# Optimization experiments

Hardware: AMD Instinct MI355X
Metric: run time of the kernel (lower is better)

## Reference

```python
import jax, jax.numpy as jnp
import numpy as np

GRID = 32            # grid_size -> num_locs = 1024
H, W = 8, 32         # ray panorama height/width
N_ANGLES = 360       # binned_rays: one bin per rounded degree


def _circ_conv(x, w, b, pad):
    # Conv2d with padding_mode='circular' (NCHW, OIHW)
    if pad > 0:
        x = jnp.pad(x, ((0, 0), (0, 0), (pad, pad), (pad, pad)), mode='wrap')
    y = jax.lax.conv_general_dilated(x, w, (1, 1), 'VALID',
                                     dimension_numbers=('NCHW', 'OIHW', 'NCHW'))
    return y + b[None, :, None, None]


def setup_inputs() -> dict:
    key = jax.random.key(0)
    ks = jax.random.split(key, 8)
    B, N, F, Co = 2, 20, 128, 64
    bbox = jax.random.uniform(ks[0], (B, 4), dtype=jnp.float32)
    near_locs = jax.random.uniform(ks[1], (B, N, 2), dtype=jnp.float32)
    near_feats = jax.random.normal(ks[2], (B, N, F, H, W), dtype=jnp.float32)
    overhead_feat = jax.random.normal(ks[3], (B, Co, GRID, GRID), dtype=jnp.float32)
    rays = jax.random.normal(ks[4], (N_ANGLES, 3, H, W), dtype=jnp.float32)
    cin = 8  # 1 dist + 3 orient + 2 pano stats + 2 overhead stats
    W1 = jax.random.normal(ks[5], (1, cin, 3, 3), dtype=jnp.float32) * 0.1
    b1 = jnp.zeros((1,), jnp.float32)
    W2 = jax.random.normal(ks[6], (1, cin, 5, 5), dtype=jnp.float32) * 0.1
    b2 = jnp.zeros((1,), jnp.float32)
    Wf = jax.random.normal(ks[7], (1, 2, 1, 1), dtype=jnp.float32) * 0.1
    bf = jnp.zeros((1,), jnp.float32)
    return dict(bbox=bbox, near_locs=near_locs, near_feats=near_feats,
                overhead_feat=overhead_feat, rays=rays,
                W1=W1, b1=b1, W2=W2, b2=b2, Wf=Wf, bf=bf)


def _grid_helper(bbox, near_locs):
    # grid-cell centers from bbox; D = euclidean dist, theta = bearing in [0, 2pi)
    ys = jnp.linspace(bbox[0], bbox[2], GRID)
    xs = jnp.linspace(bbox[1], bbox[3], GRID)
    gy, gx = jnp.meshgrid(ys, xs, indexing='ij')
    centers = jnp.stack([gy.ravel(), gx.ravel()], -1)              # [L,2]
    diff = near_locs[None, :, :] - centers[:, None, :]             # [L,N,2]
    D = jnp.sqrt(jnp.sum(diff * diff, -1))                         # [L,N]
    theta = jnp.mod(jnp.arctan2(diff[..., 1], diff[..., 0]), 2.0 * jnp.pi)
    return D, theta


def _one(bbox, near_locs, near_feats, overhead_feat, rays, W1, b1, W2, b2, Wf, bf):
    N, F = near_feats.shape[:2]
    L = GRID * GRID
    D, theta = _grid_helper(bbox, near_locs)
    theta_inds = jnp.mod(jnp.round(jnp.rad2deg(theta)).astype(jnp.int32), N_ANGLES)
    orientation = rays[theta_inds.reshape(-1)].reshape(L, N, 3, H, W)  # irregular gather
    distance = jnp.broadcast_to(D[:, :, None, None, None], (L, N, 1, H, W))
    # panorama stats: max/mean over channel dim of pano features
    pano_stats = jnp.stack([near_feats.max(1), near_feats.mean(1)], 1)  # [N,2,H,W]
    x_pano = jnp.broadcast_to(pano_stats[None], (L, N, 2, H, W))
    # overhead stats: flatten spatial -> (L, Co), max/mean over channels
    ov = overhead_feat.reshape(overhead_feat.shape[0], -1).T            # [L, Co]
    ov_stats = jnp.stack([ov.max(1), ov.mean(1)], 1)                    # [L,2]
    x_ov = jnp.broadcast_to(ov_stats[:, None, :, None, None], (L, N, 2, H, W))
    inp = jnp.concatenate([distance, orientation, x_pano, x_ov], 2)     # [L,N,8,H,W]
    x = inp.reshape(L * N, 8, H, W)
    c1 = _circ_conv(x, W1, b1, 1)
    c2 = _circ_conv(x, W2, b2, 2)
    fused = jnp.concatenate([c1, c2], 1)                                # [L*N,2,H,W]
    logits = _circ_conv(fused, Wf, bf, 0).reshape(L, N, H, W)
    weight = jax.nn.softmax(logits.reshape(L, -1), axis=1).reshape(L, N, H, W)
    tmp_feats = jnp.transpose(near_feats, (0, 2, 3, 1))                 # [N,H,W,F]
    grid_feats = jnp.einsum('pxyf,spxy->sf', tmp_feats, weight)         # [L,F]
    return (grid_feats.reshape(GRID, GRID, F),
            weight.reshape(GRID, GRID, N, H, W))


def reference(bbox, near_locs, near_feats, overhead_feat, rays, W1, b1, W2, b2, Wf, bf):
    fn = jax.vmap(_one, in_axes=(0, 0, 0, 0, None, None, None, None, None, None, None))
    return fn(bbox, near_locs, near_feats, overhead_feat, rays, W1, b1, W2, b2, Wf, bf)
```

## Files before the change

kernel.cpp:

```cpp
#include <hip/hip_runtime.h>
#include <hip/hip_fp16.h>
#include <math.h>

#define HH 8
#define WW 32
#define HW 256
#define NN 20
#define FF 128
#define LL 1024
#define AA 360
#define CO 64
#define KK 5120
#define KS 8
#define KC 640
#define BM 32
#define BK 64

#define OFF_LPANO      (AA*HW)
#define OFF_OV(B)      (OFF_LPANO + (B)*NN*HW)
#define OFF_SCAL(B)    (OFF_OV(B) + (B)*LL*2)
#define OFF_BASE(B)    (OFF_SCAL(B) + 8)
#define OFF_IDX(B)     (OFF_BASE(B) + (B)*LL*NN)
#define OFF_BT(B)      (((OFF_IDX(B) + (B)*LL*NN + 7)/8)*8)
#define OFF_CP(B)      (OFF_BT(B) + (B)*FF*KK/2)

typedef __attribute__((ext_vector_type(8))) _Float16 f16x8;
typedef __attribute__((ext_vector_type(4))) _Float16 f16x4;
typedef __attribute__((ext_vector_type(4))) float f32x4;

__global__ __launch_bounds__(256)
void k1_pre(const float* __restrict__ rays, const float* __restrict__ feats,
            const float* __restrict__ overhead,
            const float* __restrict__ W1, const float* __restrict__ b1,
            const float* __restrict__ W2, const float* __restrict__ b2,
            const float* __restrict__ Wf, const float* __restrict__ bfp,
            float* __restrict__ ws, int B)
{
    const int bid = blockIdx.x, tid = threadIdx.x;
    const float wf0 = Wf[0], wf1 = Wf[1];

    if (bid < AA) {
        __shared__ float s[3*HW];
        for (int c = 0; c < 3; ++c) s[c*HW + tid] = rays[(bid*3 + c)*HW + tid];
        __syncthreads();
        const int h = tid >> 5, w = tid & 31;
        float c1 = 0.f, c2 = 0.f;
        #pragma unroll
        for (int c = 0; c < 3; ++c) {
            #pragma unroll
            for (int ky = 0; ky < 3; ++ky)
                #pragma unroll
                for (int kx = 0; kx < 3; ++kx)
                    c1 += W1[(1+c)*9 + ky*3 + kx] *
                          s[c*HW + (((h+ky+7)&7)<<5) + ((w+kx+31)&31)];
            #pragma unroll
            for (int ky = 0; ky < 5; ++ky)
                #pragma unroll
                for (int kx = 0; kx < 5; ++kx)
                    c2 += W2[(1+c)*25 + ky*5 + kx] *
                          s[c*HW + (((h+ky+6)&7)<<5) + ((w+kx+30)&31)];
        }
        ws[bid*HW + tid] = wf0*c1 + wf1*c2;
        return;
    }

    const int pb = bid - AA;
    if (pb < B*NN) {
        __shared__ float p[2*HW];
        const float* fp = feats + (size_t)pb * FF * HW + tid;
        float mx = -INFINITY; double sm = 0.0;
        for (int f = 0; f < FF; ++f) {
            float v = fp[(size_t)f * HW];
            mx = fmaxf(mx, v); sm += (double)v;
        }
        p[tid]      = mx;
        p[HW + tid] = (float)(sm / 128.0);
        __syncthreads();
        const int h = tid >> 5, w = tid & 31;
        float c1 = 0.f, c2 = 0.f;
        #pragma unroll
        for (int c = 0; c < 2; ++c) {
            #pragma unroll
            for (int ky = 0; ky < 3; ++ky)
                #pragma unroll
                for (int kx = 0; kx < 3; ++kx)
                    c1 += W1[(4+c)*9 + ky*3 + kx] *
                          p[c*HW + (((h+ky+7)&7)<<5) + ((w+kx+31)&31)];
            #pragma unroll
            for (int ky = 0; ky < 5; ++ky)
                #pragma unroll
                for (int kx = 0; kx < 5; ++kx)
                    c2 += W2[(4+c)*25 + ky*5 + kx] *
                          p[c*HW + (((h+ky+6)&7)<<5) + ((w+kx+30)&31)];
        }
        ws[OFF_LPANO + pb*HW + tid] = wf0*c1 + wf1*c2;
        return;
    }

    const int ob = bid - AA - B*NN;
    if (ob < B*4) {
        const int t = ob*256 + tid;
        const int b = t >> 10, l = t & 1023;
        const float* op = overhead + (size_t)b*CO*LL + l;
        float mx = -INFINITY; double sm = 0.0;
        for (int c = 0; c < CO; ++c) {
            float v = op[(size_t)c*LL];
            mx = fmaxf(mx, v); sm += (double)v;
        }
        ws[OFF_OV(B) + t*2]     = mx;
        ws[OFF_OV(B) + t*2 + 1] = (float)(sm / 64.0);
        return;
    }

    if (tid == 0) {
        double s10=0, s16=0, s17=0, s20=0, s26=0, s27=0;
        for (int i = 0; i < 9;  ++i) { s10 += W1[i]; s16 += W1[54+i];  s17 += W1[63+i]; }
        for (int i = 0; i < 25; ++i) { s20 += W2[i]; s26 += W2[150+i]; s27 += W2[175+i]; }
        ws[OFF_SCAL(B)+0] = (float)(wf0*s10 + wf1*s20);
        ws[OFF_SCAL(B)+1] = (float)(wf0*s16 + wf1*s26);
        ws[OFF_SCAL(B)+2] = (float)(wf0*s17 + wf1*s27);
        ws[OFF_SCAL(B)+3] = wf0*b1[0] + wf1*b2[0] + bfp[0];
    }
}

__global__ __launch_bounds__(256)
void k2_geom(const float* __restrict__ bbox, const float* __restrict__ locs,
             float* __restrict__ ws, int B)
{
    const int t = blockIdx.x*256 + threadIdx.x;
    if (t >= B*LL*NN) return;
    const int b = t / (LL*NN), r = t % (LL*NN), l = r / NN, n = r % NN;
    const int iy = l >> 5, ix = l & 31;
    const double y0 = (double)bbox[b*4+0], x0 = (double)bbox[b*4+1];
    const double y1 = (double)bbox[b*4+2], x1 = (double)bbox[b*4+3];
    const double cy = y0 + (double)iy * (y1 - y0) / 31.0;
    const double cx = x0 + (double)ix * (x1 - x0) / 31.0;
    const double d0 = (double)locs[(b*NN+n)*2+0] - cy;
    const double d1 = (double)locs[(b*NN+n)*2+1] - cx;
    const double D  = sqrt(d0*d0 + d1*d1);
    double th = atan2(d1, d0);
    const double TWO_PI = 6.283185307179586476925286766559;
    th -= TWO_PI * floor(th / TWO_PI);
    const double deg = th * 57.295779513082320876798154814105;
    int k = (int)llrint(deg);
    int idx = k % 360; if (idx < 0) idx += 360;

    const float Cd  = ws[OFF_SCAL(B)+0], Com = ws[OFF_SCAL(B)+1];
    const float Cov = ws[OFF_SCAL(B)+2], Cb  = ws[OFF_SCAL(B)+3];
    const int bl = b*LL + l;
    const float bv = (float)(Cd * D) + Com*ws[OFF_OV(B)+bl*2]
                   + Cov*ws[OFF_OV(B)+bl*2+1] + Cb;
    ws[OFF_BASE(B) + t] = bv;
    ((int*)(ws + OFF_IDX(B)))[t] = idx;
}

__global__ __launch_bounds__(256)
void k2b_bt(const float* __restrict__ feats, float* __restrict__ ws, int B)
{
    const int NG_PER_B = NN*FF*64;
    const int g = blockIdx.x*256 + threadIdx.x;
    if (g >= B*NG_PER_B) return;
    const int b = g / NG_PER_B;
    const int r = g - b*NG_PER_B;
    const int n = r / (FF*64);
    const int r2 = r % (FF*64);
    const int f = r2 >> 6;
    const int hw0 = (r2 & 63) << 2;
    const float4 v = *(const float4*)(feats + ((size_t)((b*NN + n)*FF + f))*HW + hw0);
    f16x4 h;
    h[0] = (_Float16)v.x; h[1] = (_Float16)v.y;
    h[2] = (_Float16)v.z; h[3] = (_Float16)v.w;
    _Float16* bt = (_Float16*)(ws + OFF_BT(B));
    *(f16x4*)(bt + ((size_t)(b*FF + f))*KK + n*HW + hw0) = h;
}

__global__ __launch_bounds__(256)
void k3_softmax(const float* __restrict__ ws, float* __restrict__ out, int B)
{
    const int bid = blockIdx.x, tid = threadIdx.x;
    const int b = bid / LL;
    const float* Lray  = ws;
    const float* Lpano = ws + OFF_LPANO;
    const float* base  = ws + OFF_BASE(B) + (size_t)bid*NN;
    const int*   idxp  = (const int*)(ws + OFF_IDX(B)) + (size_t)bid*NN;

    __shared__ float sb[NN];
    __shared__ int   si[NN];
    __shared__ float sred[8];
    if (tid < NN) { sb[tid] = base[tid]; si[tid] = idxp[tid]; }
    __syncthreads();

    float lg[NN];
    float mx = -INFINITY;
    #pragma unroll
    for (int n = 0; n < NN; ++n) {
        lg[n] = sb[n] + Lray[si[n]*HW + tid] + Lpano[(b*NN+n)*HW + tid];
        mx = fmaxf(mx, lg[n]);
    }
    #pragma unroll
    for (int o = 32; o > 0; o >>= 1) mx = fmaxf(mx, __shfl_xor(mx, o, 64));
    if ((tid & 63) == 0) sred[tid >> 6] = mx;
    __syncthreads();
    mx = fmaxf(fmaxf(sred[0], sred[1]), fmaxf(sred[2], sred[3]));

    float sm = 0.f;
    #pragma unroll
    for (int n = 0; n < NN; ++n) { lg[n] = expf(lg[n] - mx); sm += lg[n]; }
    #pragma unroll
    for (int o = 32; o > 0; o >>= 1) sm += __shfl_xor(sm, o, 64);
    if ((tid & 63) == 0) sred[4 + (tid >> 6)] = sm;
    __syncthreads();
    const float inv = 1.0f / (sred[4] + sred[5] + sred[6] + sred[7]);

    float* wout = out + (size_t)B*LL*FF + (size_t)bid*NN*HW + tid;
    #pragma unroll
    for (int n = 0; n < NN; ++n) wout[n*HW] = lg[n] * inv;
}

__global__ __launch_bounds__(256)
void k4_gemm(const float* __restrict__ wbuf, const float* __restrict__ ws,
             float* __restrict__ cp, int B)
{
    __shared__ __align__(16) _Float16 As[BM*BK];
    __shared__ __align__(16) _Float16 Bs[FF*BK];
    const int x = blockIdx.x;
    const int ks = x & 7, mb = (x >> 3) & 31, b = x >> 8;
    const int l0 = mb * BM;
    const int kc0 = ks * KC;
    const int tid = threadIdx.x;
    const int wid = tid >> 6, lane = tid & 63, lr = lane & 15, lk = lane >> 4;

    const float*    Wb  = wbuf + ((size_t)(b*LL + l0))*KK;
    const _Float16* Btb = (const _Float16*)(ws + OFF_BT(B)) + (size_t)b*FF*KK;

    f32x4 acc[2][2] = {};

    int aoff[2][2], boff[2][2];
    #pragma unroll
    for (int m = 0; m < 2; ++m)
        #pragma unroll
        for (int kk = 0; kk < 2; ++kk) {
            const int row = m*16 + lr;
            aoff[m][kk] = row*128 + ((kk*64 + lk*16) ^ ((row & 7) << 4));
        }
    #pragma unroll
    for (int n = 0; n < 2; ++n)
        #pragma unroll
        for (int kk = 0; kk < 2; ++kk) {
            const int row = wid*32 + n*16 + lr;
            boff[n][kk] = row*128 + ((kk*64 + lk*16) ^ ((row & 7) << 4));
        }

    const int arow = tid >> 3, ac8 = tid & 7;
    const int adst = arow*128 + ((ac8*16) ^ ((arow & 7) << 4));

    char* AsB = (char*)As;
    char* BsB = (char*)Bs;

    for (int s = 0; s < KC/BK; ++s) {
        const int kc = kc0 + s*BK;
        {
            const float* src = Wb + (size_t)arow*KK + kc + ac8*8;
            const float4 v0 = *(const float4*)src;
            const float4 v1 = *(const float4*)(src + 4);
            f16x8 h;
            h[0] = (_Float16)v0.x; h[1] = (_Float16)v0.y;
            h[2] = (_Float16)v0.z; h[3] = (_Float16)v0.w;
            h[4] = (_Float16)v1.x; h[5] = (_Float16)v1.y;
            h[6] = (_Float16)v1.z; h[7] = (_Float16)v1.w;
            *(f16x8*)(AsB + adst) = h;
        }
        #pragma unroll
        for (int c = 0; c < 4; ++c) {
            const int e = c*256 + tid;
            const int row = e >> 3, c8 = e & 7;
            const f16x8 h = *(const f16x8*)(Btb + (size_t)row*KK + kc + c8*8);
            const int dst = row*128 + ((c8*16) ^ ((row & 7) << 4));
            *(f16x8*)(BsB + dst) = h;
        }
        __syncthreads();
        #pragma unroll
        for (int kk = 0; kk < 2; ++kk) {
            const f16x8 a0 = *(const f16x8*)(AsB + aoff[0][kk]);
            const f16x8 a1 = *(const f16x8*)(AsB + aoff[1][kk]);
            const f16x8 b0 = *(const f16x8*)(BsB + boff[0][kk]);
            const f16x8 b1 = *(const f16x8*)(BsB + boff[1][kk]);
            acc[0][0] = __builtin_amdgcn_mfma_f32_16x16x32_f16(a0, b0, acc[0][0], 0, 0, 0);
            acc[0][1] = __builtin_amdgcn_mfma_f32_16x16x32_f16(a0, b1, acc[0][1], 0, 0, 0);
            acc[1][0] = __builtin_amdgcn_mfma_f32_16x16x32_f16(a1, b0, acc[1][0], 0, 0, 0);
            acc[1][1] = __builtin_amdgcn_mfma_f32_16x16x32_f16(a1, b1, acc[1][1], 0, 0, 0);
        }
        __syncthreads();
    }

    float* cpb = cp + ((size_t)ks*B*LL + (size_t)b*LL + l0)*FF;
    #pragma unroll
    for (int m = 0; m < 2; ++m)
        #pragma unroll
        for (int n = 0; n < 2; ++n) {
            const int col = wid*32 + n*16 + lr;
            #pragma unroll
            for (int r = 0; r < 4; ++r) {
                const int row = m*16 + lk*4 + r;
                cpb[(size_t)row*FF + col] = acc[m][n][r];
            }
        }
}

__global__ __launch_bounds__(256)
void k5_reduce(const float* __restrict__ cp, float* __restrict__ gout, int B)
{
    const size_t total = (size_t)B*LL*FF;
    const size_t i = ((size_t)blockIdx.x*256 + threadIdx.x)*4;
    if (i >= total) return;
    float4 s = {0.f, 0.f, 0.f, 0.f};
    #pragma unroll
    for (int ks = 0; ks < KS; ++ks) {
        const float4 v = *(const float4*)(cp + ks*total + i);
        s.x += v.x; s.y += v.y; s.z += v.z; s.w += v.w;
    }
    *(float4*)(gout + i) = s;
}

extern "C" void kernel_launch(void* const* d_in, const int* in_sizes, int n_in,
                              void* d_out, int out_size, void* d_ws, size_t ws_size,
                              hipStream_t stream)
{
    const float* bbox  = (const float*)d_in[0];
    const float* locs  = (const float*)d_in[1];
    const float* feats = (const float*)d_in[2];
    const float* over  = (const float*)d_in[3];
    const float* rays  = (const float*)d_in[4];
    const float* W1    = (const float*)d_in[5];
    const float* b1    = (const float*)d_in[6];
    const float* W2    = (const float*)d_in[7];
    const float* b2    = (const float*)d_in[8];
    const float* Wf    = (const float*)d_in[9];
    const float* bfp   = (const float*)d_in[10];
    const int B = in_sizes[0] / 4;
    float* ws  = (float*)d_ws;
    float* out = (float*)d_out;
    float* wout = out + (size_t)B*LL*FF;
    float* cp   = ws + OFF_CP(B);

    k1_pre<<<dim3(AA + B*NN + B*4 + 1), dim3(256), 0, stream>>>(
        rays, feats, over, W1, b1, W2, b2, Wf, bfp, ws, B);
    k2_geom<<<dim3((B*LL*NN + 255)/256), dim3(256), 0, stream>>>(bbox, locs, ws, B);
    k2b_bt<<<dim3(B*NN*FF*64/256), dim3(256), 0, stream>>>(feats, ws, B);
    k3_softmax<<<dim3(B*LL), dim3(256), 0, stream>>>(ws, out, B);
    k4_gemm<<<dim3(B*32*KS), dim3(256), 0, stream>>>(wout, ws, cp, B);
    k5_reduce<<<dim3((B*LL*FF/4 + 255)/256), dim3(256), 0, stream>>>(cp, out, B);
}
```

Baseline: 43.54 us.

## Fuse softmax weight materialization into GEMM and merge prep kernels

Merges the precompute, geometry and fp16 feature-transpose kernels into a single launch. The base-logit computation moves into the softmax-stats kernel, which now stores only the per-location max and inverse sum. The GEMM kernel recomputes the softmax weights on the fly from the ray and pano logits, writes the fp32 weight output, and feeds them straight into the MFMA tiles. This avoids re-reading the full fp32 weight tensor from global memory and saves two kernel launches, at the cost of computing exp twice per element.

```diff
diff --git a/kernel.cpp b/kernel.cpp
--- a/kernel.cpp
+++ b/kernel.cpp
@@ -19,9 +19,12 @@
 #define OFF_LPANO      (AA*HW)
 #define OFF_OV(B)      (OFF_LPANO + (B)*NN*HW)
 #define OFF_SCAL(B)    (OFF_OV(B) + (B)*LL*2)
-#define OFF_BASE(B)    (OFF_SCAL(B) + 8)
-#define OFF_IDX(B)     (OFF_BASE(B) + (B)*LL*NN)
-#define OFF_BT(B)      (((OFF_IDX(B) + (B)*LL*NN + 7)/8)*8)
+#define OFF_D(B)       (OFF_SCAL(B) + 8)
+#define OFF_IDX(B)     (OFF_D(B) + (B)*LL*NN)
+#define OFF_BASE2(B)   (OFF_IDX(B) + (B)*LL*NN)
+#define OFF_MX(B)      (OFF_BASE2(B) + (B)*LL*NN)
+#define OFF_INV(B)     (OFF_MX(B) + (B)*LL)
+#define OFF_BT(B)      (((OFF_INV(B) + (B)*LL + 7)/8)*8)
 #define OFF_CP(B)      (OFF_BT(B) + (B)*FF*KK/2)
 
 typedef __attribute__((ext_vector_type(8))) _Float16 f16x8;
@@ -29,7 +32,8 @@
 typedef __attribute__((ext_vector_type(4))) float f32x4;
 
 __global__ __launch_bounds__(256)
-void k1_pre(const float* __restrict__ rays, const float* __restrict__ feats,
+void kA_pre(const float* __restrict__ bbox, const float* __restrict__ locs,
+            const float* __restrict__ rays, const float* __restrict__ feats,
             const float* __restrict__ overhead,
             const float* __restrict__ W1, const float* __restrict__ b1,
             const float* __restrict__ W2, const float* __restrict__ b2,
@@ -37,157 +41,160 @@
             float* __restrict__ ws, int B)
 {
     const int bid = blockIdx.x, tid = threadIdx.x;
-    const float wf0 = Wf[0], wf1 = Wf[1];
-
-    if (bid < AA) {
-        __shared__ float s[3*HW];
-        for (int c = 0; c < 3; ++c) s[c*HW + tid] = rays[(bid*3 + c)*HW + tid];
-        __syncthreads();
-        const int h = tid >> 5, w = tid & 31;
-        float c1 = 0.f, c2 = 0.f;
-        #pragma unroll
-        for (int c = 0; c < 3; ++c) {
+    const int g1 = AA + B*NN + B*4 + 1;
+    const int gGeo = (B*LL*NN + 255)/256;
+
+    if (bid < g1) {
+        const float wf0 = Wf[0], wf1 = Wf[1];
+
+        if (bid < AA) {
+            __shared__ float s[3*HW];
+            for (int c = 0; c < 3; ++c) s[c*HW + tid] = rays[(bid*3 + c)*HW + tid];
+            __syncthreads();
+            const int h = tid >> 5, w = tid & 31;
+            float c1 = 0.f, c2 = 0.f;
             #pragma unroll
-            for (int ky = 0; ky < 3; ++ky)
+            for (int c = 0; c < 3; ++c) {
                 #pragma unroll
-                for (int kx = 0; kx < 3; ++kx)
-                    c1 += W1[(1+c)*9 + ky*3 + kx] *
-                          s[c*HW + (((h+ky+7)&7)<<5) + ((w+kx+31)&31)];
+                for (int ky = 0; ky < 3; ++ky)
+                    #pragma unroll
+                    for (int kx = 0; kx < 3; ++kx)
+                        c1 += W1[(1+c)*9 + ky*3 + kx] *
+                              s[c*HW + (((h+ky+7)&7)<<5) + ((w+kx+31)&31)];
+                #pragma unroll
+                for (int ky = 0; ky < 5; ++ky)
+                    #pragma unroll
+                    for (int kx = 0; kx < 5; ++kx)
+                        c2 += W2[(1+c)*25 + ky*5 + kx] *
+                              s[c*HW + (((h+ky+6)&7)<<5) + ((w+kx+30)&31)];
+            }
+            ws[bid*HW + tid] = wf0*c1 + wf1*c2;
+            return;
+        }
+
+        const int pb = bid - AA;
+        if (pb < B*NN) {
+            __shared__ float p[2*HW];
+            const float* fp = feats + (size_t)pb * FF * HW + tid;
+            float mx = -INFINITY; double sm = 0.0;
+            for (int f = 0; f < FF; ++f) {
+                float v = fp[(size_t)f * HW];
+                mx = fmaxf(mx, v); sm += (double)v;
+            }
+            p[tid]      = mx;
+            p[HW + tid] = (float)(sm / 128.0);
+            __syncthreads();
+            const int h = tid >> 5, w = tid & 31;
+            float c1 = 0.f, c2 = 0.f;
             #pragma unroll
-            for (int ky = 0; ky < 5; ++ky)
+            for (int c = 0; c < 2; ++c) {
                 #pragma unroll
-                for (int kx = 0; kx < 5; ++kx)
-                    c2 += W2[(1+c)*25 + ky*5 + kx] *
-                          s[c*HW + (((h+ky+6)&7)<<5) + ((w+kx+30)&31)];
-        }
-        ws[bid*HW + tid] = wf0*c1 + wf1*c2;
+                for (int ky = 0; ky < 3; ++ky)
+                    #pragma unroll
+                    for (int kx = 0; kx < 3; ++kx)
+                        c1 += W1[(4+c)*9 + ky*3 + kx] *
+                              p[c*HW + (((h+ky+7)&7)<<5) + ((w+kx+31)&31)];
+                #pragma unroll
+                for (int ky = 0; ky < 5; ++ky)
+                    #pragma unroll
+                    for (int kx = 0; kx < 5; ++kx)
+                        c2 += W2[(4+c)*25 + ky*5 + kx] *
+                              p[c*HW + (((h+ky+6)&7)<<5) + ((w+kx+30)&31)];
+            }
+            ws[OFF_LPANO + pb*HW + tid] = wf0*c1 + wf1*c2;
+            return;
+        }
+
+        const int ob = pb - B*NN;
+        if (ob < B*4) {
+            const int t = ob*256 + tid;
+            const int b = t >> 10, l = t & 1023;
+            const float* op = overhead + (size_t)b*CO*LL + l;
+            float mx = -INFINITY; double sm = 0.0;
+            for (int c = 0; c < CO; ++c) {
+                float v = op[(size_t)c*LL];
+                mx = fmaxf(mx, v); sm += (double)v;
+            }
+            ws[OFF_OV(B) + t*2]     = mx;
+            ws[OFF_OV(B) + t*2 + 1] = (float)(sm / 64.0);
+            return;
+        }
+
+        if (tid == 0) {
+            double s10=0, s16=0, s17=0, s20=0, s26=0, s27=0;
+            for (int i = 0; i < 9;  ++i) { s10 += W1[i]; s16 += W1[54+i];  s17 += W1[63+i]; }
+            for (int i = 0; i < 25; ++i) { s20 += W2[i]; s26 += W2[150+i]; s27 += W2[175+i]; }
+            ws[OFF_SCAL(B)+0] = (float)(wf0*s10 + wf1*s20);
+            ws[OFF_SCAL(B)+1] = (float)(wf0*s16 + wf1*s26);
+            ws[OFF_SCAL(B)+2] = (float)(wf0*s17 + wf1*s27);
+            ws[OFF_SCAL(B)+3] = wf0*b1[0] + wf1*b2[0] + bfp[0];
+        }
         return;
     }
 
-    const int pb = bid - AA;
-    if (pb < B*NN) {
-        __shared__ float p[2*HW];
-        const float* fp = feats + (size_t)pb * FF * HW + tid;
-        float mx = -INFINITY; double sm = 0.0;
-        for (int f = 0; f < FF; ++f) {
-            float v = fp[(size_t)f * HW];
-            mx = fmaxf(mx, v); sm += (double)v;
-        }
-        p[tid]      = mx;
-        p[HW + tid] = (float)(sm / 128.0);
-        __syncthreads();
-        const int h = tid >> 5, w = tid & 31;
-        float c1 = 0.f, c2 = 0.f;
-        #pragma unroll
-        for (int c = 0; c < 2; ++c) {
-            #pragma unroll
-            for (int ky = 0; ky < 3; ++ky)
-                #pragma unroll
-                for (int kx = 0; kx < 3; ++kx)
-                    c1 += W1[(4+c)*9 + ky*3 + kx] *
-                          p[c*HW + (((h+ky+7)&7)<<5) + ((w+kx+31)&31)];
-            #pragma unroll
-            for (int ky = 0; ky < 5; ++ky)
-                #pragma unroll
-                for (int kx = 0; kx < 5; ++kx)
-                    c2 += W2[(4+c)*25 + ky*5 + kx] *
-                          p[c*HW + (((h+ky+6)&7)<<5) + ((w+kx+30)&31)];
-        }
-        ws[OFF_LPANO + pb*HW + tid] = wf0*c1 + wf1*c2;
+    if (bid < g1 + gGeo) {
+        const int t = (bid - g1)*256 + tid;
+        if (t >= B*LL*NN) return;
+        const int b = t / (LL*NN), r = t % (LL*NN), l = r / NN, n = r % NN;
+        const int iy = l >> 5, ix = l & 31;
+        const double y0 = (double)bbox[b*4+0], x0 = (double)bbox[b*4+1];
+        const double y1 = (double)bbox[b*4+2], x1 = (double)bbox[b*4+3];
+        const double cy = y0 + (double)iy * (y1 - y0) / 31.0;
+        const double cx = x0 + (double)ix * (x1 - x0) / 31.0;
+        const double d0 = (double)locs[(b*NN+n)*2+0] - cy;
+        const double d1 = (double)locs[(b*NN+n)*2+1] - cx;
+        const double D  = sqrt(d0*d0 + d1*d1);
+        double th = atan2(d1, d0);
+        const double TWO_PI = 6.283185307179586476925286766559;
+        th -= TWO_PI * floor(th / TWO_PI);
+        const double deg = th * 57.295779513082320876798154814105;
+        int k = (int)llrint(deg);
+        int idx = k % 360; if (idx < 0) idx += 360;
+        ws[OFF_D(B) + t] = (float)D;
+        ((int*)(ws + OFF_IDX(B)))[t] = idx;
         return;
     }
 
-    const int ob = bid - AA - B*NN;
-    if (ob < B*4) {
-        const int t = ob*256 + tid;
-        const int b = t >> 10, l = t & 1023;
-        const float* op = overhead + (size_t)b*CO*LL + l;
-        float mx = -INFINITY; double sm = 0.0;
-        for (int c = 0; c < CO; ++c) {
-            float v = op[(size_t)c*LL];
-            mx = fmaxf(mx, v); sm += (double)v;
-        }
-        ws[OFF_OV(B) + t*2]     = mx;
-        ws[OFF_OV(B) + t*2 + 1] = (float)(sm / 64.0);
-        return;
-    }
-
-    if (tid == 0) {
-        double s10=0, s16=0, s17=0, s20=0, s26=0, s27=0;
-        for (int i = 0; i < 9;  ++i) { s10 += W1[i]; s16 += W1[54+i];  s17 += W1[63+i]; }
-        for (int i = 0; i < 25; ++i) { s20 += W2[i]; s26 += W2[150+i]; s27 += W2[175+i]; }
-        ws[OFF_SCAL(B)+0] = (float)(wf0*s10 + wf1*s20);
-        ws[OFF_SCAL(B)+1] = (float)(wf0*s16 + wf1*s26);
-        ws[OFF_SCAL(B)+2] = (float)(wf0*s17 + wf1*s27);
-        ws[OFF_SCAL(B)+3] = wf0*b1[0] + wf1*b2[0] + bfp[0];
+    {
+        const int NG_PER_B = NN*FF*64;
+        const int g = (bid - g1 - gGeo)*256 + tid;
+        if (g >= B*NG_PER_B) return;
+        const int b = g / NG_PER_B;
+        const int r = g - b*NG_PER_B;
+        const int n = r / (FF*64);
+        const int r2 = r % (FF*64);
+        const int f = r2 >> 6;
+        const int hw0 = (r2 & 63) << 2;
+        const float4 v = *(const float4*)(feats + ((size_t)((b*NN + n)*FF + f))*HW + hw0);
+        f16x4 h;
+        h[0] = (_Float16)v.x; h[1] = (_Float16)v.y;
+        h[2] = (_Float16)v.z; h[3] = (_Float16)v.w;
+        _Float16* bt = (_Float16*)(ws + OFF_BT(B));
+        *(f16x4*)(bt + ((size_t)(b*FF + f))*KK + n*HW + hw0) = h;
     }
 }
 
 __global__ __launch_bounds__(256)
-void k2_geom(const float* __restrict__ bbox, const float* __restrict__ locs,
-             float* __restrict__ ws, int B)
-{
-    const int t = blockIdx.x*256 + threadIdx.x;
-    if (t >= B*LL*NN) return;
-    const int b = t / (LL*NN), r = t % (LL*NN), l = r / NN, n = r % NN;
-    const int iy = l >> 5, ix = l & 31;
-    const double y0 = (double)bbox[b*4+0], x0 = (double)bbox[b*4+1];
-    const double y1 = (double)bbox[b*4+2], x1 = (double)bbox[b*4+3];
-    const double cy = y0 + (double)iy * (y1 - y0) / 31.0;
-    const double cx = x0 + (double)ix * (x1 - x0) / 31.0;
-    const double d0 = (double)locs[(b*NN+n)*2+0] - cy;
-    const double d1 = (double)locs[(b*NN+n)*2+1] - cx;
-    const double D  = sqrt(d0*d0 + d1*d1);
-    double th = atan2(d1, d0);
-    const double TWO_PI = 6.283185307179586476925286766559;
-    th -= TWO_PI * floor(th / TWO_PI);
-    const double deg = th * 57.295779513082320876798154814105;
-    int k = (int)llrint(deg);
-    int idx = k % 360; if (idx < 0) idx += 360;
-
-    const float Cd  = ws[OFF_SCAL(B)+0], Com = ws[OFF_SCAL(B)+1];
-    const float Cov = ws[OFF_SCAL(B)+2], Cb  = ws[OFF_SCAL(B)+3];
-    const int bl = b*LL + l;
-    const float bv = (float)(Cd * D) + Com*ws[OFF_OV(B)+bl*2]
-                   + Cov*ws[OFF_OV(B)+bl*2+1] + Cb;
-    ws[OFF_BASE(B) + t] = bv;
-    ((int*)(ws + OFF_IDX(B)))[t] = idx;
-}
-
-__global__ __launch_bounds__(256)
-void k2b_bt(const float* __restrict__ feats, float* __restrict__ ws, int B)
-{
-    const int NG_PER_B = NN*FF*64;
-    const int g = blockIdx.x*256 + threadIdx.x;
-    if (g >= B*NG_PER_B) return;
-    const int b = g / NG_PER_B;
-    const int r = g - b*NG_PER_B;
-    const int n = r / (FF*64);
-    const int r2 = r % (FF*64);
-    const int f = r2 >> 6;
-    const int hw0 = (r2 & 63) << 2;
-    const float4 v = *(const float4*)(feats + ((size_t)((b*NN + n)*FF + f))*HW + hw0);
-    f16x4 h;
-    h[0] = (_Float16)v.x; h[1] = (_Float16)v.y;
-    h[2] = (_Float16)v.z; h[3] = (_Float16)v.w;
-    _Float16* bt = (_Float16*)(ws + OFF_BT(B));
-    *(f16x4*)(bt + ((size_t)(b*FF + f))*KK + n*HW + hw0) = h;
-}
-
-__global__ __launch_bounds__(256)
-void k3_softmax(const float* __restrict__ ws, float* __restrict__ out, int B)
+void kB_stats(float* __restrict__ ws, int B)
 {
     const int bid = blockIdx.x, tid = threadIdx.x;
     const int b = bid / LL;
     const float* Lray  = ws;
     const float* Lpano = ws + OFF_LPANO;
-    const float* base  = ws + OFF_BASE(B) + (size_t)bid*NN;
-    const int*   idxp  = (const int*)(ws + OFF_IDX(B)) + (size_t)bid*NN;
 
     __shared__ float sb[NN];
     __shared__ int   si[NN];
     __shared__ float sred[8];
-    if (tid < NN) { sb[tid] = base[tid]; si[tid] = idxp[tid]; }
+    if (tid < NN) {
+        const float Dv = ws[OFF_D(B) + (size_t)bid*NN + tid];
+        const int   ix = ((const int*)(ws + OFF_IDX(B)))[(size_t)bid*NN + tid];
+        const float Cd  = ws[OFF_SCAL(B)+0], Com = ws[OFF_SCAL(B)+1];
+        const float Cov = ws[OFF_SCAL(B)+2], Cb  = ws[OFF_SCAL(B)+3];
+        const float bv = Cd*Dv + Com*ws[OFF_OV(B)+bid*2]
+                       + Cov*ws[OFF_OV(B)+bid*2+1] + Cb;
+        sb[tid] = bv; si[tid] = ix;
+        ws[OFF_BASE2(B) + (size_t)bid*NN + tid] = bv;
+    }
     __syncthreads();
 
     float lg[NN];
@@ -205,32 +212,49 @@
 
     float sm = 0.f;
     #pragma unroll
-    for (int n = 0; n < NN; ++n) { lg[n] = expf(lg[n] - mx); sm += lg[n]; }
+    for (int n = 0; n < NN; ++n) sm += expf(lg[n] - mx);
     #pragma unroll
     for (int o = 32; o > 0; o >>= 1) sm += __shfl_xor(sm, o, 64);
     if ((tid & 63) == 0) sred[4 + (tid >> 6)] = sm;
     __syncthreads();
-    const float inv = 1.0f / (sred[4] + sred[5] + sred[6] + sred[7]);
-
-    float* wout = out + (size_t)B*LL*FF + (size_t)bid*NN*HW + tid;
-    #pragma unroll
-    for (int n = 0; n < NN; ++n) wout[n*HW] = lg[n] * inv;
+    if (tid == 0) {
+        ws[OFF_MX(B)  + bid] = mx;
+        ws[OFF_INV(B) + bid] = 1.0f / (sred[4] + sred[5] + sred[6] + sred[7]);
+    }
 }
 
 __global__ __launch_bounds__(256)
-void k4_gemm(const float* __restrict__ wbuf, const float* __restrict__ ws,
+void kC_gemm(const float* __restrict__ ws, float* __restrict__ wout,
              float* __restrict__ cp, int B)
 {
     __shared__ __align__(16) _Float16 As[BM*BK];
     __shared__ __align__(16) _Float16 Bs[FF*BK];
+    __shared__ float smx[BM], sinv[BM], sbase[BM*3];
+    __shared__ int   sidx2[BM*3];
+
     const int x = blockIdx.x;
     const int ks = x & 7, mb = (x >> 3) & 31, b = x >> 8;
     const int l0 = mb * BM;
     const int kc0 = ks * KC;
+    const int n0 = kc0 >> 8;
+    const int bl0 = b*LL + l0;
     const int tid = threadIdx.x;
     const int wid = tid >> 6, lane = tid & 63, lr = lane & 15, lk = lane >> 4;
 
-    const float*    Wb  = wbuf + ((size_t)(b*LL + l0))*KK;
+    if (tid < BM) {
+        smx[tid]  = ws[OFF_MX(B)  + bl0 + tid];
+        sinv[tid] = ws[OFF_INV(B) + bl0 + tid];
+    } else if (tid >= 64 && tid < 64 + BM*3) {
+        const int t = tid - 64;
+        const int row = t/3, jj = t - row*3, n = n0 + jj;
+        float bv = 0.f; int ix = 0;
+        if (n < NN) {
+            bv = ws[OFF_BASE2(B) + (size_t)(bl0 + row)*NN + n];
+            ix = ((const int*)(ws + OFF_IDX(B)))[(size_t)(bl0 + row)*NN + n];
+        }
+        sbase[t] = bv; sidx2[t] = ix;
+    }
+
     const _Float16* Btb = (const _Float16*)(ws + OFF_BT(B)) + (size_t)b*FF*KK;
 
     f32x4 acc[2][2] = {};
@@ -257,17 +281,40 @@
     char* AsB = (char*)As;
     char* BsB = (char*)Bs;
 
+    __syncthreads();
+
     for (int s = 0; s < KC/BK; ++s) {
         const int kc = kc0 + s*BK;
+        const int n = kc >> 8, jj = n - n0;
         {
-            const float* src = Wb + (size_t)arow*KK + kc + ac8*8;
-            const float4 v0 = *(const float4*)src;
-            const float4 v1 = *(const float4*)(src + 4);
+            const int hwt = (kc & 255) + ac8*8;
+            const float* lrp = ws + (size_t)sidx2[arow*3 + jj]*HW + hwt;
+            const float* lpp = ws + OFF_LPANO + (size_t)(b*NN + n)*HW + hwt;
+            const float bb = sbase[arow*3 + jj];
+            const float m  = smx[arow];
+            const float iv = sinv[arow];
+            const float4 r0 = *(const float4*)lrp;
+            const float4 r1 = *(const float4*)(lrp + 4);
+            const float4 p0 = *(const float4*)lpp;
+            const float4 p1 = *(const float4*)(lpp + 4);
+            float w0 = expf(((bb + r0.x) + p0.x) - m) * iv;
+            float w1 = expf(((bb + r0.y) + p0.y) - m) * iv;
+            float w2 = expf(((bb + r0.z) + p0.z) - m) * iv;
+            float w3 = expf(((bb + r0.w) + p0.w) - m) * iv;
+            float w4 = expf(((bb + r1.x) + p1.x) - m) * iv;
+            float w5 = expf(((bb + r1.y) + p1.y) - m) * iv;
+            float w6 = expf(((bb + r1.z) + p1.z) - m) * iv;
+            float w7 = expf(((bb + r1.w) + p1.w) - m) * iv;
+            float* wp = wout + (size_t)(bl0 + arow)*KK + kc + ac8*8;
+            const float4 o0 = {w0, w1, w2, w3};
+            const float4 o1 = {w4, w5, w6, w7};
+            *(float4*)wp = o0;
+            *(float4*)(wp + 4) = o1;
             f16x8 h;
-            h[0] = (_Float16)v0.x; h[1] = (_Float16)v0.y;
-            h[2] = (_Float16)v0.z; h[3] = (_Float16)v0.w;
-            h[4] = (_Float16)v1.x; h[5] = (_Float16)v1.y;
-            h[6] = (_Float16)v1.z; h[7] = (_Float16)v1.w;
+            h[0] = (_Float16)w0; h[1] = (_Float16)w1;
+            h[2] = (_Float16)w2; h[3] = (_Float16)w3;
+            h[4] = (_Float16)w4; h[5] = (_Float16)w5;
+            h[6] = (_Float16)w6; h[7] = (_Float16)w7;
             *(f16x8*)(AsB + adst) = h;
         }
         #pragma unroll
@@ -293,7 +340,7 @@
         __syncthreads();
     }
 
-    float* cpb = cp + ((size_t)ks*B*LL + (size_t)b*LL + l0)*FF;
+    float* cpb = cp + ((size_t)ks*B*LL + (size_t)bl0)*FF;
     #pragma unroll
     for (int m = 0; m < 2; ++m)
         #pragma unroll
@@ -308,7 +355,7 @@
 }
 
 __global__ __launch_bounds__(256)
-void k5_reduce(const float* __restrict__ cp, float* __restrict__ gout, int B)
+void kD_reduce(const float* __restrict__ cp, float* __restrict__ gout, int B)
 {
     const size_t total = (size_t)B*LL*FF;
     const size_t i = ((size_t)blockIdx.x*256 + threadIdx.x)*4;
@@ -343,11 +390,13 @@
     float* wout = out + (size_t)B*LL*FF;
     float* cp   = ws + OFF_CP(B);
 
-    k1_pre<<<dim3(AA + B*NN + B*4 + 1), dim3(256), 0, stream>>>(
-        rays, feats, over, W1, b1, W2, b2, Wf, bfp, ws, B);
-    k2_geom<<<dim3((B*LL*NN + 255)/256), dim3(256), 0, stream>>>(bbox, locs, ws, B);
-    k2b_bt<<<dim3(B*NN*FF*64/256), dim3(256), 0, stream>>>(feats, ws, B);
-    k3_softmax<<<dim3(B*LL), dim3(256), 0, stream>>>(ws, out, B);
-    k4_gemm<<<dim3(B*32*KS), dim3(256), 0, stream>>>(wout, ws, cp, B);
-    k5_reduce<<<dim3((B*LL*FF/4 + 255)/256), dim3(256), 0, stream>>>(cp, out, B);
+    const int g1   = AA + B*NN + B*4 + 1;
+    const int gGeo = (B*LL*NN + 255)/256;
+    const int gBt  = (B*NN*FF*64)/256;
+
+    kA_pre<<<dim3(g1 + gGeo + gBt), dim3(256), 0, stream>>>(
+        bbox, locs, rays, feats, over, W1, b1, W2, b2, Wf, bfp, ws, B);
+    kB_stats<<<dim3(B*LL), dim3(256), 0, stream>>>(ws, B);
+    kC_gemm<<<dim3(B*32*KS), dim3(256), 0, stream>>>(ws, wout, cp, B);
+    kD_reduce<<<dim3((B*LL*FF/4 + 255)/256), dim3(256), 0, stream>>>(cp, out, B);
 }
```

Result: no change. 43.64 us (+0.2%).
